# Optimization experiments

Hardware: AMD Instinct MI355X
Metric: run time of the kernel (lower is better)

## Reference

```python
import jax, jax.numpy as jnp
import numpy as np

B, L, D, DEG = 32, 1024, 512, 8
E = B * L * DEG  # 262144 edges total
N = B * L


def setup_inputs() -> dict:
    key = jax.random.key(0)
    ks = jax.random.split(key, 8)
    text_feature = jax.random.normal(ks[0], (B, L, D), jnp.float32)
    # edge list per sample (torch.nonzero(edge_matrix[i]) equivalent), offset by b*L like PyG batching
    src_local = jax.random.randint(ks[1], (E,), 0, L, jnp.int32)
    dst_local = jax.random.randint(ks[2], (E,), 0, L, jnp.int32)
    boff = (jnp.arange(E, dtype=jnp.int32) // (E // B)) * L
    edge_src = src_local + boff
    edge_dst = dst_local + boff
    s = 1.0 / np.sqrt(D)
    W1 = jax.random.uniform(ks[3], (D, D), jnp.float32, -s, s)   # node Linear
    b1 = jax.random.uniform(ks[4], (D,), jnp.float32, -s, s)
    gamma = jnp.ones((D,), jnp.float32)      # BatchNorm1d weight
    beta = jnp.zeros((D,), jnp.float32)      # BatchNorm1d bias
    run_mean = jnp.zeros((D,), jnp.float32)  # BN running stats (eval mode)
    run_var = jnp.ones((D,), jnp.float32)
    alpha1 = jnp.array(0.25, jnp.float32)    # PReLU (node MLP)
    Wg = jax.random.uniform(ks[5], (D, D), jnp.float32, -s, s)   # GCNConv lin (bias=False)
    bg = jnp.zeros((D,), jnp.float32)        # GCNConv bias
    alpha2 = jnp.array(0.25, jnp.float32)    # PReLU (after GCN)
    return {"text_feature": text_feature, "edge_src": edge_src, "edge_dst": edge_dst,
            "W1": W1, "b1": b1, "gamma": gamma, "beta": beta,
            "run_mean": run_mean, "run_var": run_var, "alpha1": alpha1,
            "Wg": Wg, "bg": bg, "alpha2": alpha2}


def reference(text_feature, edge_src, edge_dst, W1, b1, gamma, beta,
              run_mean, run_var, alpha1, Wg, bg, alpha2):
    Bs, Ls, Ds = text_feature.shape
    Nn = Bs * Ls
    xf = text_feature.reshape(Nn, Ds)
    # node MLP: Linear -> BatchNorm1d (eval) -> PReLU
    h = xf @ W1 + b1
    h = (h - run_mean) * jax.lax.rsqrt(run_var + 1e-5) * gamma + beta
    h = jnp.where(h >= 0, h, alpha1 * h)
    # GCNConv: add self loops, symmetric degree norm, gather->scatter-add, + bias
    nodes = jnp.arange(Nn, dtype=edge_src.dtype)
    src = jnp.concatenate([edge_src, nodes])
    dst = jnp.concatenate([edge_dst, nodes])
    deg = jnp.zeros((Nn,), h.dtype).at[dst].add(1.0)  # in-degree incl. self loop, >= 1
    dinv = jax.lax.rsqrt(deg)
    xw = h @ Wg                               # [N, D]
    msg = (xw * dinv[:, None])[src]           # gather D^{-1/2}-scaled messages [E+N, D]
    agg = jnp.zeros_like(xw).at[dst].add(msg) * dinv[:, None]
    g = agg + bg
    g = jnp.where(g >= 0, g, alpha2 * g)      # PReLU
    g = g.reshape(Bs, Ls, Ds)
    # F.normalize(p=2, dim=2) + residual (original input)
    g = g / jnp.clip(jnp.linalg.norm(g, axis=2, keepdims=True), 1e-12)
    return g + text_feature
```

## Files before the change

### kernel.cpp

```cpp
#include <hip/hip_runtime.h>
#include <math.h>

#define DD    512
#define NN    32768
#define EE    262144

typedef float f32x4 __attribute__((ext_vector_type(4)));
typedef __bf16 bf16x8 __attribute__((ext_vector_type(8)));
typedef __bf16 bf16x4 __attribute__((ext_vector_type(4)));

__global__ void k_zero(int* __restrict__ cnt) {
    int i = blockIdx.x * 256 + threadIdx.x;
    if (i < NN) cnt[i] = 0;
}

__global__ void k_count(const int* __restrict__ dst, int* __restrict__ cnt) {
    int e = blockIdx.x * 256 + threadIdx.x;
    if (e < EE) atomicAdd(&cnt[dst[e]], 1);
}

__global__ __launch_bounds__(1024) void k_scan(
    const int* __restrict__ cnt, int* __restrict__ offs,
    int* __restrict__ cursor, float* __restrict__ dinv)
{
    __shared__ int part[1024];
    int t = threadIdx.x;
    int base = t * 32;
    int local[32];
    int s = 0;
#pragma unroll
    for (int i = 0; i < 32; ++i) { local[i] = s; s += cnt[base + i]; }
    part[t] = s;
    __syncthreads();
    for (int off = 1; off < 1024; off <<= 1) {
        int v = (t >= off) ? part[t - off] : 0;
        __syncthreads();
        part[t] += v;
        __syncthreads();
    }
    int prev = (t == 0) ? 0 : part[t - 1];
#pragma unroll
    for (int i = 0; i < 32; ++i) {
        int o = prev + local[i];
        offs[base + i] = o;
        cursor[base + i] = o;
        dinv[base + i] = rsqrtf((float)cnt[base + i] + 1.0f);
    }
    if (t == 1023) offs[NN] = part[1023];
}

__global__ void k_fill(const int* __restrict__ src, const int* __restrict__ dst,
                       int* __restrict__ cursor, int* __restrict__ csr) {
    int e = blockIdx.x * 256 + threadIdx.x;
    if (e < EE) {
        int d = dst[e];
        int p = atomicAdd(&cursor[d], 1);
        csr[p] = src[e];
    }
}

__global__ __launch_bounds__(256) void k_cvt(const float* __restrict__ in, __bf16* __restrict__ out) {
    int i = blockIdx.x * 256 + threadIdx.x;
    float4 v = ((const float4*)in)[i];
    bf16x4 o;
    o[0] = (__bf16)v.x; o[1] = (__bf16)v.y; o[2] = (__bf16)v.z; o[3] = (__bf16)v.w;
    *(bf16x4*)(out + (size_t)i * 4) = o;
}

__global__ __launch_bounds__(256) void k_wt(const float* __restrict__ W1, const float* __restrict__ Wg,
                                            __bf16* __restrict__ W1t, __bf16* __restrict__ Wgt) {
    __shared__ float tile[32][33];
    const float* W = blockIdx.z ? Wg : W1;
    __bf16* Wt = blockIdx.z ? Wgt : W1t;
    int x0 = blockIdx.x * 32;
    int y0 = blockIdx.y * 32;
    int tx = threadIdx.x;
    for (int j = threadIdx.y; j < 32; j += 8)
        tile[j][tx] = W[(size_t)(y0 + j) * DD + x0 + tx];
    __syncthreads();
    for (int j = threadIdx.y; j < 32; j += 8)
        Wt[(size_t)(x0 + j) * DD + y0 + tx] = (__bf16)tile[tx][j];
}

template <int MODE>
__global__ __launch_bounds__(256) void k_gemm_mfma(
    const __bf16* __restrict__ A,
    const __bf16* __restrict__ Bt,
    __bf16* __restrict__ Cout,
    const float* __restrict__ bias,
    const float* __restrict__ gamma, const float* __restrict__ beta,
    const float* __restrict__ mean, const float* __restrict__ var,
    const float* __restrict__ alphap,
    const float* __restrict__ dinv)
{
    __shared__ __bf16 lds[2][128 * 32];

    const int tid  = threadIdx.x;
    const int lane = tid & 63;
    const int w    = tid >> 6;
    const int wm   = (w >> 1) * 64;
    const int wn   = (w & 1) * 64;
    const int m0   = blockIdx.x * 128;
    const int n0   = blockIdx.y * 128;

    f32x4 acc[4][4] = {};

    for (int k0 = 0; k0 < DD; k0 += 32) {
        __syncthreads();
#pragma unroll
        for (int rd = 0; rd < 2; ++rd) {
            int cbase = rd * 256 + w * 64;
            int cidx = cbase + lane;
            int r = cidx >> 2, s = cidx & 3;
            int c = s ^ ((r >> 1) & 3);
            const __bf16* ga = A  + (size_t)(m0 + r) * DD + k0 + c * 8;
            const __bf16* gb = Bt + (size_t)(n0 + r) * DD + k0 + c * 8;
            __builtin_amdgcn_global_load_lds(
                (const __attribute__((address_space(1))) unsigned int*)ga,
                (__attribute__((address_space(3))) unsigned int*)(&lds[0][cbase * 8]), 16, 0, 0);
            __builtin_amdgcn_global_load_lds(
                (const __attribute__((address_space(1))) unsigned int*)gb,
                (__attribute__((address_space(3))) unsigned int*)(&lds[1][cbase * 8]), 16, 0, 0);
        }
        __syncthreads();

        bf16x8 af[4], bf[4];
#pragma unroll
        for (int m = 0; m < 4; ++m) {
            int r = wm + m * 16 + (lane & 15);
            int s = (lane >> 4) ^ ((r >> 1) & 3);
            af[m] = *(const bf16x8*)&lds[0][r * 32 + s * 8];
            int q = wn + m * 16 + (lane & 15);
            int sq = (lane >> 4) ^ ((q >> 1) & 3);
            bf[m] = *(const bf16x8*)&lds[1][q * 32 + sq * 8];
        }
#pragma unroll
        for (int m = 0; m < 4; ++m)
#pragma unroll
            for (int n = 0; n < 4; ++n)
                acc[m][n] = __builtin_amdgcn_mfma_f32_16x16x32_bf16(af[m], bf[n], acc[m][n], 0, 0, 0);
    }

    float alpha = (MODE == 1) ? alphap[0] : 0.0f;
#pragma unroll
    for (int m = 0; m < 4; ++m) {
        int row_base = m0 + wm + m * 16 + ((lane >> 4) << 2);
#pragma unroll
        for (int n = 0; n < 4; ++n) {
            int col = n0 + wn + n * 16 + (lane & 15);
#pragma unroll
            for (int j = 0; j < 4; ++j) {
                int row = row_base + j;
                float x = acc[m][n][j];
                if (MODE == 1) {
                    x += bias[col];
                    x = (x - mean[col]) * rsqrtf(var[col] + 1e-5f) * gamma[col] + beta[col];
                    x = (x >= 0.0f) ? x : alpha * x;
                } else {
                    x *= dinv[row];
                }
                Cout[(size_t)row * DD + col] = (__bf16)x;
            }
        }
    }
}

__global__ __launch_bounds__(128) void k_gather_final(
    const int* __restrict__ offs, const int* __restrict__ csr,
    const __bf16* __restrict__ xws, const float* __restrict__ dinv,
    const float* __restrict__ bg, const float* __restrict__ alpha2,
    const float* __restrict__ text, float* __restrict__ out)
{
    int blk = blockIdx.x;
    int node = ((blk & 7) << 12) + (blk >> 3);
    int t = threadIdx.x;
    int c = t * 4;
    int beg = offs[node], end = offs[node + 1];

    bf16x4 sv = *(const bf16x4*)(xws + (size_t)node * DD + c);
    float a0 = (float)sv[0], a1 = (float)sv[1], a2v = (float)sv[2], a3 = (float)sv[3];
    for (int e = beg; e < end; ++e) {
        int s = csr[e];
        bf16x4 v = *(const bf16x4*)(xws + (size_t)s * DD + c);
        a0 += (float)v[0]; a1 += (float)v[1]; a2v += (float)v[2]; a3 += (float)v[3];
    }

    float di = dinv[node];
    float al = alpha2[0];
    float4 bgv = *(const float4*)(bg + c);
    float g0 = a0 * di + bgv.x;
    float g1 = a1 * di + bgv.y;
    float g2 = a2v * di + bgv.z;
    float g3 = a3 * di + bgv.w;
    g0 = (g0 >= 0.0f) ? g0 : al * g0;
    g1 = (g1 >= 0.0f) ? g1 : al * g1;
    g2 = (g2 >= 0.0f) ? g2 : al * g2;
    g3 = (g3 >= 0.0f) ? g3 : al * g3;

    float ss = g0 * g0 + g1 * g1 + g2 * g2 + g3 * g3;
#pragma unroll
    for (int off = 32; off > 0; off >>= 1) ss += __shfl_down(ss, off, 64);
    __shared__ float red[2];
    if ((t & 63) == 0) red[t >> 6] = ss;
    __syncthreads();
    float inv = 1.0f / fmaxf(sqrtf(red[0] + red[1]), 1e-12f);

    float4 tx = *(const float4*)(text + (size_t)node * DD + c);
    float4 o;
    o.x = g0 * inv + tx.x;
    o.y = g1 * inv + tx.y;
    o.z = g2 * inv + tx.z;
    o.w = g3 * inv + tx.w;
    *(float4*)(out + (size_t)node * DD + c) = o;
}

extern "C" void kernel_launch(void* const* d_in, const int* in_sizes, int n_in,
                              void* d_out, int out_size, void* d_ws, size_t ws_size,
                              hipStream_t stream) {
    const float* text   = (const float*)d_in[0];
    const int*   esrc   = (const int*)d_in[1];
    const int*   edst   = (const int*)d_in[2];
    const float* W1     = (const float*)d_in[3];
    const float* b1     = (const float*)d_in[4];
    const float* gamma  = (const float*)d_in[5];
    const float* beta   = (const float*)d_in[6];
    const float* rmean  = (const float*)d_in[7];
    const float* rvar   = (const float*)d_in[8];
    const float* alpha1 = (const float*)d_in[9];
    const float* Wg     = (const float*)d_in[10];
    const float* bg     = (const float*)d_in[11];
    const float* alpha2 = (const float*)d_in[12];
    float* out = (float*)d_out;

    char* p = (char*)d_ws;
    auto alloc = [&](size_t bytes) { char* r = p; p += (bytes + 255) & ~(size_t)255; return r; };
    int*    cnt     = (int*)alloc((size_t)NN * 4);
    int*    offs    = (int*)alloc((size_t)(NN + 1) * 4);
    int*    cursor  = (int*)alloc((size_t)NN * 4);
    float*  dinv    = (float*)alloc((size_t)NN * 4);
    int*    csr     = (int*)alloc((size_t)EE * 4);
    __bf16* W1t     = (__bf16*)alloc((size_t)DD * DD * 2);
    __bf16* Wgt     = (__bf16*)alloc((size_t)DD * DD * 2);
    __bf16* h_bf    = (__bf16*)alloc((size_t)NN * DD * 2);
    __bf16* text_bf = (__bf16*)alloc((size_t)NN * DD * 2);
    __bf16* xws     = (__bf16*)alloc((size_t)NN * DD * 2);

    k_zero<<<NN / 256, 256, 0, stream>>>(cnt);
    k_count<<<EE / 256, 256, 0, stream>>>(edst, cnt);
    k_scan<<<1, 1024, 0, stream>>>(cnt, offs, cursor, dinv);
    k_fill<<<EE / 256, 256, 0, stream>>>(esrc, edst, cursor, csr);

    k_cvt<<<(NN * DD / 4) / 256, 256, 0, stream>>>(text, text_bf);
    k_wt<<<dim3(16, 16, 2), dim3(32, 8), 0, stream>>>(W1, Wg, W1t, Wgt);

    dim3 gg(NN / 128, DD / 128);
    k_gemm_mfma<1><<<gg, 256, 0, stream>>>(text_bf, W1t, h_bf, b1, gamma, beta, rmean, rvar, alpha1, nullptr);

    k_gemm_mfma<2><<<gg, 256, 0, stream>>>(h_bf, Wgt, xws, nullptr, nullptr, nullptr, nullptr, nullptr, nullptr, dinv);

    k_gather_final<<<NN, 128, 0, stream>>>(offs, csr, xws, dinv, bg, alpha2, text, out);
}
```

Measured before the change: 173.2 us.

## Fuse fp32-to-bf16 input conversion into GEMM, reorder grid, widen gather per wave

The separate text fp32-to-bf16 conversion kernel is removed. GEMM1 now loads fp32 rows directly, converts them in registers and stores them to LDS, which drops one pass over the activation and the bf16 intermediate buffer. The GEMM grid is reordered so the four N-tiles sharing an M-block run adjacently, improving L2 reuse of the A rows. The gather kernel now assigns one wave per node with 8 channels per lane, unrolls neighbours by 4 for memory-level parallelism, and uses a wave-only xor reduction instead of shared memory. The trade-off is that GEMM1's A loads become synchronous register loads rather than async global-to-LDS copies, and each tile reads twice the bytes.

```diff
diff --git a/kernel.cpp b/kernel.cpp
--- a/kernel.cpp
+++ b/kernel.cpp
@@ -57,14 +57,6 @@
         int p = atomicAdd(&cursor[d], 1);
         csr[p] = src[e];
     }
-}
-
-__global__ __launch_bounds__(256) void k_cvt(const float* __restrict__ in, __bf16* __restrict__ out) {
-    int i = blockIdx.x * 256 + threadIdx.x;
-    float4 v = ((const float4*)in)[i];
-    bf16x4 o;
-    o[0] = (__bf16)v.x; o[1] = (__bf16)v.y; o[2] = (__bf16)v.z; o[3] = (__bf16)v.w;
-    *(bf16x4*)(out + (size_t)i * 4) = o;
 }
 
 __global__ __launch_bounds__(256) void k_wt(const float* __restrict__ W1, const float* __restrict__ Wg,
@@ -84,7 +76,7 @@
 
 template <int MODE>
 __global__ __launch_bounds__(256) void k_gemm_mfma(
-    const __bf16* __restrict__ A,
+    const void* __restrict__ Ap,
     const __bf16* __restrict__ Bt,
     __bf16* __restrict__ Cout,
     const float* __restrict__ bias,
@@ -100,8 +92,8 @@
     const int w    = tid >> 6;
     const int wm   = (w >> 1) * 64;
     const int wn   = (w & 1) * 64;
-    const int m0   = blockIdx.x * 128;
-    const int n0   = blockIdx.y * 128;
+    const int n0   = blockIdx.x * 128;
+    const int m0   = blockIdx.y * 128;
 
     f32x4 acc[4][4] = {};
 
@@ -113,14 +105,39 @@
             int cidx = cbase + lane;
             int r = cidx >> 2, s = cidx & 3;
             int c = s ^ ((r >> 1) & 3);
-            const __bf16* ga = A  + (size_t)(m0 + r) * DD + k0 + c * 8;
             const __bf16* gb = Bt + (size_t)(n0 + r) * DD + k0 + c * 8;
-            __builtin_amdgcn_global_load_lds(
-                (const __attribute__((address_space(1))) unsigned int*)ga,
-                (__attribute__((address_space(3))) unsigned int*)(&lds[0][cbase * 8]), 16, 0, 0);
             __builtin_amdgcn_global_load_lds(
                 (const __attribute__((address_space(1))) unsigned int*)gb,
                 (__attribute__((address_space(3))) unsigned int*)(&lds[1][cbase * 8]), 16, 0, 0);
+        }
+        if constexpr (MODE == 1) {
+            const float* A = (const float*)Ap;
+#pragma unroll
+            for (int hh = 0; hh < 2; ++hh) {
+                int ci = tid + hh * 256;
+                int r = ci >> 2, s = ci & 3;
+                int c = s ^ ((r >> 1) & 3);
+                const float* ga = A + (size_t)(m0 + r) * DD + k0 + c * 8;
+                float4 f0 = *(const float4*)ga;
+                float4 f1 = *(const float4*)(ga + 4);
+                bf16x8 o;
+                o[0] = (__bf16)f0.x; o[1] = (__bf16)f0.y; o[2] = (__bf16)f0.z; o[3] = (__bf16)f0.w;
+                o[4] = (__bf16)f1.x; o[5] = (__bf16)f1.y; o[6] = (__bf16)f1.z; o[7] = (__bf16)f1.w;
+                *(bf16x8*)&lds[0][ci * 8] = o;
+            }
+        } else {
+            const __bf16* A = (const __bf16*)Ap;
+#pragma unroll
+            for (int rd = 0; rd < 2; ++rd) {
+                int cbase = rd * 256 + w * 64;
+                int cidx = cbase + lane;
+                int r = cidx >> 2, s = cidx & 3;
+                int c = s ^ ((r >> 1) & 3);
+                const __bf16* ga = A + (size_t)(m0 + r) * DD + k0 + c * 8;
+                __builtin_amdgcn_global_load_lds(
+                    (const __attribute__((address_space(1))) unsigned int*)ga,
+                    (__attribute__((address_space(3))) unsigned int*)(&lds[0][cbase * 8]), 16, 0, 0);
+            }
         }
         __syncthreads();
 
@@ -165,53 +182,71 @@
     }
 }
 
-__global__ __launch_bounds__(128) void k_gather_final(
+__global__ __launch_bounds__(256) void k_gather_final(
     const int* __restrict__ offs, const int* __restrict__ csr,
     const __bf16* __restrict__ xws, const float* __restrict__ dinv,
     const float* __restrict__ bg, const float* __restrict__ alpha2,
     const float* __restrict__ text, float* __restrict__ out)
 {
     int blk = blockIdx.x;
-    int node = ((blk & 7) << 12) + (blk >> 3);
-    int t = threadIdx.x;
-    int c = t * 4;
+    int sb  = ((blk & 7) << 10) + (blk >> 3);
+    int wave = threadIdx.x >> 6;
+    int lane = threadIdx.x & 63;
+    int node = sb * 4 + wave;
+    int c = lane * 8;
     int beg = offs[node], end = offs[node + 1];
-
-    bf16x4 sv = *(const bf16x4*)(xws + (size_t)node * DD + c);
-    float a0 = (float)sv[0], a1 = (float)sv[1], a2v = (float)sv[2], a3 = (float)sv[3];
-    for (int e = beg; e < end; ++e) {
-        int s = csr[e];
-        bf16x4 v = *(const bf16x4*)(xws + (size_t)s * DD + c);
-        a0 += (float)v[0]; a1 += (float)v[1]; a2v += (float)v[2]; a3 += (float)v[3];
+    int ne = end - beg;
+
+    bf16x8 sv = *(const bf16x8*)(xws + (size_t)node * DD + c);
+    float a[8];
+#pragma unroll
+    for (int i = 0; i < 8; ++i) a[i] = (float)sv[i];
+
+    int k = 0;
+    for (; k + 4 <= ne; k += 4) {
+        int s0 = csr[beg + k + 0];
+        int s1 = csr[beg + k + 1];
+        int s2 = csr[beg + k + 2];
+        int s3 = csr[beg + k + 3];
+        bf16x8 v0 = *(const bf16x8*)(xws + (size_t)s0 * DD + c);
+        bf16x8 v1 = *(const bf16x8*)(xws + (size_t)s1 * DD + c);
+        bf16x8 v2 = *(const bf16x8*)(xws + (size_t)s2 * DD + c);
+        bf16x8 v3 = *(const bf16x8*)(xws + (size_t)s3 * DD + c);
+#pragma unroll
+        for (int i = 0; i < 8; ++i)
+            a[i] += (float)v0[i] + (float)v1[i] + (float)v2[i] + (float)v3[i];
+    }
+    for (; k < ne; ++k) {
+        int s = csr[beg + k];
+        bf16x8 v = *(const bf16x8*)(xws + (size_t)s * DD + c);
+#pragma unroll
+        for (int i = 0; i < 8; ++i) a[i] += (float)v[i];
     }
 
     float di = dinv[node];
     float al = alpha2[0];
-    float4 bgv = *(const float4*)(bg + c);
-    float g0 = a0 * di + bgv.x;
-    float g1 = a1 * di + bgv.y;
-    float g2 = a2v * di + bgv.z;
-    float g3 = a3 * di + bgv.w;
-    g0 = (g0 >= 0.0f) ? g0 : al * g0;
-    g1 = (g1 >= 0.0f) ? g1 : al * g1;
-    g2 = (g2 >= 0.0f) ? g2 : al * g2;
-    g3 = (g3 >= 0.0f) ? g3 : al * g3;
-
-    float ss = g0 * g0 + g1 * g1 + g2 * g2 + g3 * g3;
-#pragma unroll
-    for (int off = 32; off > 0; off >>= 1) ss += __shfl_down(ss, off, 64);
-    __shared__ float red[2];
-    if ((t & 63) == 0) red[t >> 6] = ss;
-    __syncthreads();
-    float inv = 1.0f / fmaxf(sqrtf(red[0] + red[1]), 1e-12f);
-
-    float4 tx = *(const float4*)(text + (size_t)node * DD + c);
-    float4 o;
-    o.x = g0 * inv + tx.x;
-    o.y = g1 * inv + tx.y;
-    o.z = g2 * inv + tx.z;
-    o.w = g3 * inv + tx.w;
-    *(float4*)(out + (size_t)node * DD + c) = o;
+    float g[8];
+    float ss = 0.0f;
+#pragma unroll
+    for (int i = 0; i < 8; ++i) {
+        float x = a[i] * di + bg[c + i];
+        x = (x >= 0.0f) ? x : al * x;
+        g[i] = x;
+        ss += x * x;
+    }
+#pragma unroll
+    for (int off = 1; off < 64; off <<= 1) ss += __shfl_xor(ss, off, 64);
+    float inv = 1.0f / fmaxf(sqrtf(ss), 1e-12f);
+
+    float4 t0 = *(const float4*)(text + (size_t)node * DD + c);
+    float4 t1 = *(const float4*)(text + (size_t)node * DD + c + 4);
+    float4 o0, o1;
+    o0.x = g[0] * inv + t0.x; o0.y = g[1] * inv + t0.y;
+    o0.z = g[2] * inv + t0.z; o0.w = g[3] * inv + t0.w;
+    o1.x = g[4] * inv + t1.x; o1.y = g[5] * inv + t1.y;
+    o1.z = g[6] * inv + t1.z; o1.w = g[7] * inv + t1.w;
+    *(float4*)(out + (size_t)node * DD + c)     = o0;
+    *(float4*)(out + (size_t)node * DD + c + 4) = o1;
 }
 
 extern "C" void kernel_launch(void* const* d_in, const int* in_sizes, int n_in,
@@ -242,7 +277,6 @@
     __bf16* W1t     = (__bf16*)alloc((size_t)DD * DD * 2);
     __bf16* Wgt     = (__bf16*)alloc((size_t)DD * DD * 2);
     __bf16* h_bf    = (__bf16*)alloc((size_t)NN * DD * 2);
-    __bf16* text_bf = (__bf16*)alloc((size_t)NN * DD * 2);
     __bf16* xws     = (__bf16*)alloc((size_t)NN * DD * 2);
 
     k_zero<<<NN / 256, 256, 0, stream>>>(cnt);
@@ -250,13 +284,12 @@
     k_scan<<<1, 1024, 0, stream>>>(cnt, offs, cursor, dinv);
     k_fill<<<EE / 256, 256, 0, stream>>>(esrc, edst, cursor, csr);
 
-    k_cvt<<<(NN * DD / 4) / 256, 256, 0, stream>>>(text, text_bf);
     k_wt<<<dim3(16, 16, 2), dim3(32, 8), 0, stream>>>(W1, Wg, W1t, Wgt);
 
-    dim3 gg(NN / 128, DD / 128);
-    k_gemm_mfma<1><<<gg, 256, 0, stream>>>(text_bf, W1t, h_bf, b1, gamma, beta, rmean, rvar, alpha1, nullptr);
+    dim3 gg(DD / 128, NN / 128);
+    k_gemm_mfma<1><<<gg, 256, 0, stream>>>(text, W1t, h_bf, b1, gamma, beta, rmean, rvar, alpha1, nullptr);
 
     k_gemm_mfma<2><<<gg, 256, 0, stream>>>(h_bf, Wgt, xws, nullptr, nullptr, nullptr, nullptr, nullptr, nullptr, dinv);
 
-    k_gather_final<<<NN, 128, 0, stream>>>(offs, csr, xws, dinv, bg, alpha2, text, out);
-}
+    k_gather_final<<<NN / 4, 256, 0, stream>>>(offs, csr, xws, dinv, bg, alpha2, text, out);
+}
```

Result: faster. 165.9 us (-4.2%).
